# Optimization experiments

Hardware: AMD Instinct MI355X
Metric: run time of the kernel (lower is better)

The kernel has to match this reference:

```python
import jax, jax.numpy as jnp
import numpy as np

B, S, DIN, D, H, DK, FF, V, L = 4, 1024, 768, 224, 8, 28, 600, 8000, 8


def setup_inputs() -> dict:
    key = jax.random.key(0)
    ks = iter(jax.random.split(key, 32))
    g = lambda shape, s=0.02: jax.random.normal(next(ks), shape, jnp.float32) * s
    return {
        "x": jax.random.normal(next(ks), (B, S, DIN), jnp.float32),
        "Wp": g((DIN, D)), "bp": jnp.zeros((D,), jnp.float32),
        # per-layer stacked params, leading axis = L layers
        "Wq": g((L, H, D, DK)), "bq": jnp.zeros((L, H, DK), jnp.float32),
        "Wk": g((L, H, D, DK)), "bk": jnp.zeros((L, H, DK), jnp.float32),
        "Wv": g((L, H, D, DK)), "bv": jnp.zeros((L, H, DK), jnp.float32),
        "Wo": g((L, D, D)), "bo": jnp.zeros((L, D), jnp.float32),
        "W1": g((L, D, FF)), "b1": jnp.zeros((L, FF), jnp.float32),
        "W2": g((L, FF, FF)), "b2": jnp.zeros((L, FF), jnp.float32),
        "W3": g((L, FF, D)), "b3": jnp.zeros((L, D), jnp.float32),
        # LayerNorm over last TWO dims (seq, dmodel), one shared instance per layer
        "lnw": jnp.ones((L, S, D), jnp.float32), "lnb": jnp.zeros((L, S, D), jnp.float32),
        "Wf": g((D, V)), "bf": jnp.zeros((V,), jnp.float32),
    }


def _pos_enc(S_, D_):
    pos = jnp.arange(S_, dtype=jnp.float32)[:, None]          # [S,1]
    i = jnp.arange(D_, dtype=jnp.float32)[None, :]            # [1,D]
    ang = pos / jnp.power(jnp.float32(10000.0), 2.0 * i / D_)  # uses 2*i for BOTH
    return jnp.where(jnp.arange(D_)[None, :] % 2 == 0, jnp.sin(ang), jnp.cos(ang))


def _ln2d(x, w, b):
    # LayerNorm over last two dims (seq, dmodel), eps=1e-5
    mu = jnp.mean(x, axis=(-2, -1), keepdims=True)
    var = jnp.var(x, axis=(-2, -1), keepdims=True)
    return (x - mu) / jnp.sqrt(var + 1e-5) * w + b


def _attn(x, Wq, bq, Wk, bk, Wv, bv, Wo, bo):
    q = jnp.einsum('bsd,hdk->bhsk', x, Wq) + bq[:, None, :]
    k = jnp.einsum('bsd,hdk->bhsk', x, Wk) + bk[:, None, :]
    v = jnp.einsum('bsd,hdk->bhsk', x, Wv) + bv[:, None, :]
    scores = jnp.einsum('bhqk,bhsk->bhqs', q, k) / jnp.sqrt(jnp.float32(DK))
    causal = jnp.tril(jnp.ones((S, S), bool))
    scores = jnp.where(causal, scores, -jnp.inf)
    a = jax.nn.softmax(scores, axis=-1)
    o = jnp.einsum('bhqs,bhsk->bqhk', a, v).reshape(x.shape[0], S, D)
    return o @ Wo + bo + x  # residual inside attention (as in source)


def reference(x, Wp, bp, Wq, bq, Wk, bk, Wv, bv, Wo, bo,
              W1, b1, W2, b2, W3, b3, lnw, lnb, Wf, bf):
    h = x @ Wp + bp                      # proj_to_224: [B,S,224]
    h = h + _pos_enc(S, D)[None]         # positional encoding
    for l in range(L):
        h = _attn(h, Wq[l], bq[l], Wk[l], bk[l], Wv[l], bv[l], Wo[l], bo[l])
        h = _ln2d(h, lnw[l], lnb[l])
        f = jax.nn.relu(h @ W1[l] + b1[l])
        f = jax.nn.relu(f @ W2[l] + b2[l])
        f = f @ W3[l] + b3[l]
        h = _ln2d(f + h, lnw[l], lnb[l])  # feed_forward's LN (same params)
        h = _ln2d(h, lnw[l], lnb[l])      # outer LN (same params again)
    logits = (h @ Wf + bf) / 1.0          # temperature = 1.0
    return jax.nn.softmax(logits, axis=2)
```

## Files before the change

### kernel.cpp

```cpp
#include <hip/hip_runtime.h>
#include <math.h>

#define GF_BIAS   1
#define GF_RELU   2
#define GF_RESID  4
#define GF_POSENC 8
#define GF_F32OUT 16
#define GF_STAT6  32
#define GF_SWAP   64
#define GF_LNA    128
#define GF_LNA2   256
#define GF_LNRES  512
#define GF_LNRES2 1024

namespace {
constexpr int BB = 4, SS = 1024, DD = 224, FFF = 600, VV = 8000, LLl = 8;
constexpr int SD = SS * DD;
constexpr float INV_SD = 1.0f / (float)SD;

constexpr size_t WP   = 0;
constexpr size_t WQKV = WP + (size_t)256 * 768;
constexpr size_t WO   = WQKV + (size_t)LLl * 704 * 256;
constexpr size_t W1T  = WO + (size_t)LLl * 256 * 256;
constexpr size_t W2T  = W1T + (size_t)LLl * 640 * 256;
constexpr size_t W3T  = W2T + (size_t)LLl * 640 * 640;
constexpr size_t WFT  = W3T + (size_t)LLl * 256 * 640;
constexpr size_t HB   = WFT + (size_t)8064 * 256;
constexpr size_t H2B  = HB + (size_t)4096 * 256;
constexpr size_t OBUF = H2B + (size_t)4096 * 256;
constexpr size_t BIG  = OBUF + (size_t)4096 * 256;
constexpr size_t ENDB = BIG + (size_t)2 * 4096 * 640;
constexpr size_t FBYTE = ENDB * 2;
}

using short8 = __attribute__((ext_vector_type(8))) short;
using f32x4  = __attribute__((ext_vector_type(4))) float;

__device__ __forceinline__ float bits2f(unsigned u) {
  union { unsigned u; float f; } v; v.u = u; return v.f;
}
__device__ __forceinline__ unsigned short f2b(float f) {
  union { float f; unsigned u; } v; v.f = f;
  unsigned r = v.u + 0x7FFFu + ((v.u >> 16) & 1u);
  return (unsigned short)(r >> 16);
}
__device__ __forceinline__ float b2f(unsigned short b) {
  return bits2f((unsigned)b << 16);
}

__device__ __forceinline__ uint4 ln8(uint4 raw, const float* __restrict__ wp,
                                     const float* __restrict__ bp,
                                     float mu1, float rs1, float mu2, float rs2,
                                     bool dbl) {
  float4 w0 = *(const float4*)wp, w1v = *(const float4*)(wp + 4);
  float4 b0 = *(const float4*)bp, b1v = *(const float4*)(bp + 4);
  float wv[8] = {w0.x, w0.y, w0.z, w0.w, w1v.x, w1v.y, w1v.z, w1v.w};
  float bv[8] = {b0.x, b0.y, b0.z, b0.w, b1v.x, b1v.y, b1v.z, b1v.w};
  const unsigned* u = (const unsigned*)&raw;
  uint4 out;
  unsigned* ou = (unsigned*)&out;
#pragma unroll
  for (int q = 0; q < 4; ++q) {
    float x0 = bits2f(u[q] << 16), x1 = bits2f(u[q] & 0xFFFF0000u);
    float y0 = (x0 - mu1) * rs1 * wv[q * 2] + bv[q * 2];
    float y1 = (x1 - mu1) * rs1 * wv[q * 2 + 1] + bv[q * 2 + 1];
    if (dbl) {
      y0 = (y0 - mu2) * rs2 * wv[q * 2] + bv[q * 2];
      y1 = (y1 - mu2) * rs2 * wv[q * 2 + 1] + bv[q * 2 + 1];
    }
    ou[q] = (unsigned)f2b(y0) | ((unsigned)f2b(y1) << 16);
  }
  return out;
}

template <int BM, int BN, int FLAGS>
__global__ __launch_bounds__(256) void gemm_mfma(
    const unsigned short* __restrict__ A, const unsigned short* __restrict__ Bt,
    const float* __restrict__ bias, const unsigned short* __restrict__ Rz,
    void* __restrict__ Cout, int Kp, int N, int ldc,
    const float* __restrict__ lnwT, const float* __restrict__ lnbT,
    const float* __restrict__ stIn, const float* __restrict__ cst,
    const float* __restrict__ lnwS, const float* __restrict__ lnbS,
    float* __restrict__ statOut)
{
  constexpr bool HASLNA = (FLAGS & (GF_LNA | GF_LNA2)) != 0;
  constexpr bool HASLNR = (FLAGS & (GF_LNRES | GF_LNRES2)) != 0;
  constexpr bool DBLA = (FLAGS & GF_LNA2) != 0;
  constexpr bool DBLR = (FLAGS & GF_LNRES2) != 0;
  constexpr int MR = BM / 32, NR = BN / 32;
  constexpr int APT = BM / 32, BPT = BN / 32;
  constexpr int ABY = BM * 128, BBY = BN * 128;
  constexpr int CBY = (FLAGS & GF_F32OUT) ? (64 * (BN + 4) * 4) : (BM * (BN + 8) * 2);
  constexpr int SBY = (ABY + BBY) > CBY ? (ABY + BBY) : CBY;
  __shared__ __align__(16) char smem[SBY];
  __shared__ float red6[24];
  unsigned short* sA = (unsigned short*)smem;
  unsigned short* sB = (unsigned short*)(smem + ABY);
  const int t = threadIdx.x;
  const int l = t & 63;
  const int w = t >> 6, wr = w >> 1, wc = w & 1;
  const int m0 = ((FLAGS & GF_SWAP) ? blockIdx.x : blockIdx.y) * BM;
  const int n0 = ((FLAGS & GF_SWAP) ? blockIdx.y : blockIdx.x) * BN;
  const int nk = Kp >> 6;

  float mu1 = 0.f, rs1 = 1.f, mu2 = 0.f, rs2 = 1.f;
  if constexpr (HASLNA || HASLNR) {
    const float* st = stIn + (m0 >> 10) * 6;
    const float s0 = st[0], s1 = st[1];
    mu1 = s0 * INV_SD;
    rs1 = rsqrtf(s1 * INV_SD - mu1 * mu1 + 1e-5f);
    if constexpr (DBLA || DBLR) {
      const float swx = st[2], sw2x = st[3], sw2x2 = st[4], swbx = st[5];
      mu2 = (rs1 * (swx - mu1 * cst[0]) + cst[2]) * INV_SD;
      const float ey2 = (rs1 * rs1 * (sw2x2 - 2.f * mu1 * sw2x + mu1 * mu1 * cst[1]) +
                         2.f * rs1 * (swbx - mu1 * cst[4]) + cst[3]) * INV_SD;
      rs2 = rsqrtf(ey2 - mu2 * mu2 + 1e-5f);
    }
  }

  int aoff[APT], ar[APT], ac[APT];
#pragma unroll
  for (int p = 0; p < APT; ++p) {
    int off = (t + p * 256) * 16;
    int r = off >> 7;
    int cb = (off & 127) ^ ((r & 7) << 4);
    aoff[p] = off; ar[p] = r; ac[p] = cb >> 1;
  }
  int boff[BPT], br[BPT], bc[BPT];
#pragma unroll
  for (int p = 0; p < BPT; ++p) {
    int off = (t + p * 256) * 16;
    int r = off >> 7;
    int cb = (off & 127) ^ ((r & 7) << 4);
    boff[p] = off; br[p] = r; bc[p] = cb >> 1;
  }

  const unsigned short* Ab = A + (size_t)m0 * Kp;
  const unsigned short* Bb = Bt + (size_t)n0 * Kp;

  auto loadA = [&](int p, int kb) -> uint4 {
    const int d0 = kb + ac[p];
    uint4 raw = *(const uint4*)(Ab + (size_t)ar[p] * Kp + d0);
    if constexpr (HASLNA) {
      if (d0 >= DD) return make_uint4(0u, 0u, 0u, 0u);
      const int srow = (m0 + ar[p]) & (SS - 1);
      raw = ln8(raw, lnwT + (size_t)srow * DD + d0, lnbT + (size_t)srow * DD + d0,
                mu1, rs1, mu2, rs2, DBLA);
    }
    return raw;
  };

  uint4 ra[APT], rb[BPT];
#pragma unroll
  for (int p = 0; p < APT; ++p) ra[p] = loadA(p, 0);
#pragma unroll
  for (int p = 0; p < BPT; ++p) rb[p] = *(const uint4*)(Bb + (size_t)br[p] * Kp + bc[p]);

  f32x4 acc[MR][NR];
#pragma unroll
  for (int i = 0; i < MR; ++i)
#pragma unroll
    for (int j = 0; j < NR; ++j) acc[i][j] = {0.f, 0.f, 0.f, 0.f};

  for (int kt = 0; kt < nk; ++kt) {
#pragma unroll
    for (int p = 0; p < APT; ++p) *(uint4*)((char*)sA + aoff[p]) = ra[p];
#pragma unroll
    for (int p = 0; p < BPT; ++p) *(uint4*)((char*)sB + boff[p]) = rb[p];
    __syncthreads();
    if (kt + 1 < nk) {
      const int k1 = (kt + 1) * 64;
#pragma unroll
      for (int p = 0; p < APT; ++p) ra[p] = loadA(p, k1);
#pragma unroll
      for (int p = 0; p < BPT; ++p) rb[p] = *(const uint4*)(Bb + (size_t)br[p] * Kp + k1 + bc[p]);
    }
#pragma unroll
    for (int kh = 0; kh < 2; ++kh) {
      short8 af[MR], bfg[NR];
#pragma unroll
      for (int mi = 0; mi < MR; ++mi) {
        const int row = wr * (BM / 2) + mi * 16 + (l & 15);
        const int byte = (row * 128 + kh * 64 + (l >> 4) * 16) ^ ((row & 7) << 4);
        af[mi] = *(const short8*)((const char*)sA + byte);
      }
#pragma unroll
      for (int ni = 0; ni < NR; ++ni) {
        const int row = wc * (BN / 2) + ni * 16 + (l & 15);
        const int byte = (row * 128 + kh * 64 + (l >> 4) * 16) ^ ((row & 7) << 4);
        bfg[ni] = *(const short8*)((const char*)sB + byte);
      }
#pragma unroll
      for (int mi = 0; mi < MR; ++mi)
#pragma unroll
        for (int ni = 0; ni < NR; ++ni)
          acc[mi][ni] = __builtin_amdgcn_mfma_f32_16x16x32_bf16(af[mi], bfg[ni], acc[mi][ni], 0, 0, 0);
    }
    __syncthreads();
  }

  const int cl = l & 15, rl0 = (l >> 4) * 4;

  if constexpr ((FLAGS & GF_F32OUT) != 0) {
    constexpr int CST = BN + 4;
    float* Cs = (float*)smem;
    constexpr int NCH = BM / 64;
#pragma unroll
    for (int c = 0; c < NCH; ++c) {
      __syncthreads();
      if ((wr * (BM / 2)) / 64 == c) {
#pragma unroll
        for (int mi = 0; mi < MR; ++mi)
#pragma unroll
          for (int ni = 0; ni < NR; ++ni)
#pragma unroll
            for (int j = 0; j < 4; ++j) {
              const int rl = wr * (BM / 2) + mi * 16 + rl0 + j - c * 64;
              const int cc = wc * (BN / 2) + ni * 16 + cl;
              const int gn = n0 + cc;
              float v = acc[mi][ni][j];
              if ((FLAGS & GF_BIAS) && gn < N) v += bias[gn];
              Cs[rl * CST + cc] = v;
            }
      }
      __syncthreads();
      constexpr int CPR = BN / 4;
      constexpr int NIT = (64 * CPR) / 256;
#pragma unroll
      for (int i = 0; i < NIT; ++i) {
        const int ch = i * 256 + t;
        const int rr = ch / CPR, c4 = ch % CPR;
        const int gn = n0 + c4 * 4;
        const size_t gmr = (size_t)(m0 + c * 64 + rr);
        if (gn + 3 < N) {
          *(float4*)&((float*)Cout)[gmr * ldc + gn] = *(const float4*)&Cs[rr * CST + c4 * 4];
        } else {
#pragma unroll
          for (int c2 = 0; c2 < 4; ++c2)
            if (gn + c2 < N) ((float*)Cout)[gmr * ldc + gn + c2] = Cs[rr * CST + c4 * 4 + c2];
        }
      }
    }
  } else {
    constexpr int CST = BN + 8;
    unsigned short* Cs = (unsigned short*)smem;
    float ls0 = 0.f, ls1 = 0.f, ls2 = 0.f, ls3 = 0.f, ls4 = 0.f, ls5 = 0.f;
#pragma unroll
    for (int mi = 0; mi < MR; ++mi)
#pragma unroll
      for (int ni = 0; ni < NR; ++ni)
#pragma unroll
        for (int j = 0; j < 4; ++j) {
          const int rl = wr * (BM / 2) + mi * 16 + rl0 + j;
          const int cc = wc * (BN / 2) + ni * 16 + cl;
          const int gm = m0 + rl, gn = n0 + cc;
          const int srow = gm & (SS - 1);
          float v = acc[mi][ni][j];
          if ((FLAGS & GF_BIAS) && gn < N) v += bias[gn];
          if constexpr ((FLAGS & GF_RESID) != 0) {
            if constexpr (HASLNR) {
              if (gn < N) {
                float rv = b2f(Rz[(size_t)gm * ldc + gn]);
                const float wE = lnwT[(size_t)srow * DD + gn];
                const float bE = lnbT[(size_t)srow * DD + gn];
                rv = (rv - mu1) * rs1 * wE + bE;
                if constexpr (DBLR) rv = (rv - mu2) * rs2 * wE + bE;
                v += rv;
              }
            } else {
              v += b2f(Rz[(size_t)gm * ldc + gn]);
            }
          }
          if ((FLAGS & GF_POSENC) && gn < N) {
            float freq = expf(-(2.0f * gn / 224.0f) * 9.210340371976184f);
            float ang = (float)srow * freq;
            v += (gn & 1) ? cosf(ang) : sinf(ang);
          }
          if (FLAGS & GF_RELU) v = fmaxf(v, 0.f);
          if constexpr ((FLAGS & GF_STAT6) != 0) {
            if (gn < N) {
              const float wS = lnwS[(size_t)srow * DD + gn];
              const float bS = lnbS[(size_t)srow * DD + gn];
              const float wv = wS * v;
              ls0 += v; ls1 += v * v; ls2 += wv; ls3 += wS * wv;
              ls4 += wv * wv; ls5 += bS * wv;
            }
          }
          Cs[rl * CST + cc] = f2b(v);
        }
    __syncthreads();
#pragma unroll
    for (int it = 0; it < BM / 32; ++it) {
      const int rr = it * 32 + (t >> 3), qq = t & 7;
      const size_t gm = (size_t)(m0 + rr);
      *(uint4*)&((unsigned short*)Cout)[gm * ldc + n0 + qq * 8] =
          *(const uint4*)&Cs[rr * CST + qq * 8];
    }
    if constexpr ((FLAGS & GF_STAT6) != 0) {
      float s[6] = {ls0, ls1, ls2, ls3, ls4, ls5};
#pragma unroll
      for (int o2 = 32; o2 > 0; o2 >>= 1)
#pragma unroll
        for (int j = 0; j < 6; ++j) s[j] += __shfl_down(s[j], o2);
      if (l == 0)
#pragma unroll
        for (int j = 0; j < 6; ++j) red6[w * 6 + j] = s[j];
      __syncthreads();
      if (t < 6) {
        const float tot = red6[t] + red6[6 + t] + red6[12 + t] + red6[18 + t];
        atomicAdd(&statOut[(m0 >> 10) * 6 + t], tot);
      }
    }
  }
}

__global__ void zero_stats(float* __restrict__ st)
{
  if (threadIdx.x < 424) st[threadIdx.x] = 0.f;
}

__global__ __launch_bounds__(256) void lnconst(const float* __restrict__ lnw,
                                               const float* __restrict__ lnb,
                                               float* __restrict__ cst)
{
  const int ll = blockIdx.y, g = blockIdx.x;
  const float* wv = lnw + (size_t)ll * SD + g * 3584;
  const float* bv = lnb + (size_t)ll * SD + g * 3584;
  float s[5] = {0.f, 0.f, 0.f, 0.f, 0.f};
  for (int c = threadIdx.x * 4; c < 3584; c += 1024) {
    float4 w4 = *(const float4*)(wv + c);
    float4 b4 = *(const float4*)(bv + c);
    const float* wf = (const float*)&w4;
    const float* bf2 = (const float*)&b4;
#pragma unroll
    for (int e = 0; e < 4; ++e) {
      const float ww = wf[e], bb = bf2[e];
      s[0] += ww; s[1] += ww * ww; s[2] += bb; s[3] += bb * bb; s[4] += ww * bb;
    }
  }
#pragma unroll
  for (int o2 = 32; o2 > 0; o2 >>= 1)
#pragma unroll
    for (int j = 0; j < 5; ++j) s[j] += __shfl_down(s[j], o2);
  __shared__ float red[4][5];
  if ((threadIdx.x & 63) == 0)
#pragma unroll
    for (int j = 0; j < 5; ++j) red[threadIdx.x >> 6][j] = s[j];
  __syncthreads();
  if (threadIdx.x < 5) {
    const float tot = red[0][threadIdx.x] + red[1][threadIdx.x] +
                      red[2][threadIdx.x] + red[3][threadIdx.x];
    atomicAdd(&cst[ll * 5 + threadIdx.x], tot);
  }
}

__global__ __launch_bounds__(256) void ln2mat(
    const unsigned short* __restrict__ X, const float* __restrict__ lnw,
    const float* __restrict__ lnb, const float* __restrict__ st,
    const float* __restrict__ cst, unsigned short* __restrict__ Y)
{
  const int chunk = blockIdx.x * 256 + threadIdx.x;
  const int r = chunk >> 5, cc = chunk & 31;
  if (cc >= 28) {
    *(uint4*)(Y + (size_t)r * 256 + cc * 8) = make_uint4(0u, 0u, 0u, 0u);
    return;
  }
  const int b = r >> 10, srow = r & 1023;
  const float* s = st + b * 6;
  const float mu1 = s[0] * INV_SD;
  const float rs1 = rsqrtf(s[1] * INV_SD - mu1 * mu1 + 1e-5f);
  const float mu2 = (rs1 * (s[2] - mu1 * cst[0]) + cst[2]) * INV_SD;
  const float ey2 = (rs1 * rs1 * (s[4] - 2.f * mu1 * s[3] + mu1 * mu1 * cst[1]) +
                     2.f * rs1 * (s[5] - mu1 * cst[4]) + cst[3]) * INV_SD;
  const float rs2 = rsqrtf(ey2 - mu2 * mu2 + 1e-5f);
  uint4 raw = *(const uint4*)(X + (size_t)r * 256 + cc * 8);
  uint4 out = ln8(raw, lnw + (size_t)srow * DD + cc * 8, lnb + (size_t)srow * DD + cc * 8,
                  mu1, rs1, mu2, rs2, true);
  *(uint4*)(Y + (size_t)r * 256 + cc * 8) = out;
}

__global__ __launch_bounds__(256) void prep_wt2(
    const float* __restrict__ W, unsigned short* __restrict__ O,
    int K, int N, int Kp, int Np, size_t sW, size_t sO)
{
  const int ll = blockIdx.y;
  const int tx = Np >> 5;
  const int tn = blockIdx.x % tx, tk = blockIdx.x / tx;
  const int n0 = tn * 32, k0 = tk * 32;
  const float* Wl = W + sW * ll;
  unsigned short* Ol = O + sO * ll;
  __shared__ float T[32][36];
  {
    const int r = threadIdx.x >> 3, c4 = (threadIdx.x & 7) * 4;
    const int k = k0 + r, n = n0 + c4;
    float4 v = make_float4(0.f, 0.f, 0.f, 0.f);
    if (k < K) {
      if (n + 3 < N) v = *(const float4*)&Wl[(size_t)k * N + n];
      else {
        if (n + 0 < N) v.x = Wl[(size_t)k * N + n + 0];
        if (n + 1 < N) v.y = Wl[(size_t)k * N + n + 1];
        if (n + 2 < N) v.z = Wl[(size_t)k * N + n + 2];
        if (n + 3 < N) v.w = Wl[(size_t)k * N + n + 3];
      }
    }
    *(float4*)&T[r][c4] = v;
  }
  __syncthreads();
  {
    const int nl = threadIdx.x >> 3, k4 = (threadIdx.x & 7) * 4;
    ushort4 u;
    u.x = f2b(T[k4 + 0][nl]); u.y = f2b(T[k4 + 1][nl]);
    u.z = f2b(T[k4 + 2][nl]); u.w = f2b(T[k4 + 3][nl]);
    *(ushort4*)&Ol[(size_t)(n0 + nl) * Kp + k0 + k4] = u;
  }
}

__global__ void prep_wqkv(const float* __restrict__ Wq, const float* __restrict__ Wk,
                          const float* __restrict__ Wv, const float* __restrict__ bq,
                          const float* __restrict__ bk, const float* __restrict__ bv,
                          unsigned short* __restrict__ O, float* __restrict__ bcat)
{
  const int idx = blockIdx.x * 256 + threadIdx.x;
  if (idx < LLl * 8 * 224 * 28) {
    const int kk = idx % 28;
    const int d  = (idx / 28) % 224;
    const int h  = (idx / (28 * 224)) % 8;
    const int ll = idx / (28 * 224 * 8);
    const int col = h * 28 + kk;
    const size_t base = (size_t)ll * (704 * 256);
    O[base + (size_t)col * 256 + d]         = f2b(Wq[idx]);
    O[base + (size_t)(224 + col) * 256 + d] = f2b(Wk[idx]);
    O[base + (size_t)(448 + col) * 256 + d] = f2b(Wv[idx]);
  }
  if (idx < LLl * 8 * 28) {
    const int kk = idx % 28;
    const int h  = (idx / 28) % 8;
    const int ll = idx / (28 * 8);
    const int col = h * 28 + kk;
    bcat[ll * 672 + col]       = bq[idx];
    bcat[ll * 672 + 224 + col] = bk[idx];
    bcat[ll * 672 + 448 + col] = bv[idx];
  }
}

__global__ void prep_x(const float* __restrict__ x, unsigned short* __restrict__ xb)
{
  const size_t i = ((size_t)blockIdx.x * 256 + threadIdx.x) * 4;
  float4 v = *(const float4*)(x + i);
  ushort4 o;
  o.x = f2b(v.x); o.y = f2b(v.y); o.z = f2b(v.z); o.w = f2b(v.w);
  *(ushort4*)(xb + i) = o;
}

__global__ __launch_bounds__(256) void attn_mfma(const unsigned short* __restrict__ qkv,
                                                 unsigned short* __restrict__ o)
{
  const int bh = blockIdx.x;
  const int qt = (int)gridDim.y - 1 - (int)blockIdx.y;
  const int b = bh >> 3, h = bh & 7;
  const int tid = threadIdx.x;
  const int w = tid >> 6, l = tid & 63;
  const int cl = l & 15, g = l >> 4;
  const int qbase = qt * 64 + w * 16;
  const float scale = 0.1889822365046136f;

  __shared__ unsigned short Ks[32 * 40];
  __shared__ unsigned short Vt[32 * 40];
  __shared__ unsigned short Ps[4][16 * 40];

  short8 aq;
  {
    const unsigned short* qp = qkv + ((size_t)(b * SS + qbase + cl)) * 704 + h * 28;
#pragma unroll
    for (int e = 0; e < 8; ++e) {
      const int d = g * 8 + e;
      ((unsigned short*)&aq)[e] = (d < 28) ? qp[d] : (unsigned short)0;
    }
  }

  f32x4 o0 = {0.f, 0.f, 0.f, 0.f}, o1 = {0.f, 0.f, 0.f, 0.f};
  float m[4] = {-INFINITY, -INFINITY, -INFINITY, -INFINITY};
  float lsum[4] = {0.f, 0.f, 0.f, 0.f};

  const int ntiles = qt * 2 + 2;
  const int ntw = ((qbase + 15) >> 5) + 1;

  const int sr = tid >> 3, sc4 = (tid & 7) << 2;
  const bool sact = (sc4 < 28);
  ushort4 ku = make_ushort4(0, 0, 0, 0), vu = make_ushort4(0, 0, 0, 0);
  if (sact) {
    const unsigned short* kp = qkv + ((size_t)(b * SS + sr)) * 704 + 224 + h * 28 + sc4;
    ku = *(const ushort4*)kp;
    vu = *(const ushort4*)(kp + 224);
  }

  for (int tile = 0; tile < ntiles; ++tile) {
    const int t0 = tile * 32;
    __syncthreads();
    *(ushort4*)&Ks[sr * 40 + sc4] = ku;
    Vt[(sc4 + 0) * 40 + sr] = vu.x;
    Vt[(sc4 + 1) * 40 + sr] = vu.y;
    Vt[(sc4 + 2) * 40 + sr] = vu.z;
    Vt[(sc4 + 3) * 40 + sr] = vu.w;
    __syncthreads();
    if (tile + 1 < ntiles && sact) {
      const unsigned short* kp =
          qkv + ((size_t)(b * SS + (tile + 1) * 32 + sr)) * 704 + 224 + h * 28 + sc4;
      ku = *(const ushort4*)kp;
      vu = *(const ushort4*)(kp + 224);
    }
    if (tile >= ntw) continue;

    const short8 bk0 = *(const short8*)&Ks[cl * 40 + g * 8];
    const short8 bk1 = *(const short8*)&Ks[(cl + 16) * 40 + g * 8];
    f32x4 zz = {0.f, 0.f, 0.f, 0.f};
    f32x4 s0 = __builtin_amdgcn_mfma_f32_16x16x32_bf16(aq, bk0, zz, 0, 0, 0);
    f32x4 s1 = __builtin_amdgcn_mfma_f32_16x16x32_bf16(aq, bk1, zz, 0, 0, 0);

    const bool diag = (t0 + 31 > qbase);
#pragma unroll
    for (int jj = 0; jj < 4; ++jj) {
      float v0 = s0[jj] * scale, v1 = s1[jj] * scale;
      if (diag) {
        const int qr = qbase + g * 4 + jj;
        if (t0 + cl > qr)      v0 = -INFINITY;
        if (t0 + 16 + cl > qr) v1 = -INFINITY;
      }
      float rm = fmaxf(v0, v1);
      rm = fmaxf(rm, __shfl_xor(rm, 1));
      rm = fmaxf(rm, __shfl_xor(rm, 2));
      rm = fmaxf(rm, __shfl_xor(rm, 4));
      rm = fmaxf(rm, __shfl_xor(rm, 8));
      const float mnew = fmaxf(m[jj], rm);
      const float r2 = __expf(m[jj] - mnew);
      m[jj] = mnew;
      const float e0 = __expf(v0 - mnew), e1 = __expf(v1 - mnew);
      lsum[jj] = lsum[jj] * r2 + e0 + e1;
      o0[jj] *= r2; o1[jj] *= r2;
      Ps[w][(g * 4 + jj) * 40 + cl]      = f2b(e0);
      Ps[w][(g * 4 + jj) * 40 + cl + 16] = f2b(e1);
    }
    const short8 pa  = *(const short8*)&Ps[w][cl * 40 + g * 8];
    const short8 bv0 = *(const short8*)&Vt[cl * 40 + g * 8];
    const short8 bv1 = *(const short8*)&Vt[(cl + 16) * 40 + g * 8];
    o0 = __builtin_amdgcn_mfma_f32_16x16x32_bf16(pa, bv0, o0, 0, 0, 0);
    o1 = __builtin_amdgcn_mfma_f32_16x16x32_bf16(pa, bv1, o1, 0, 0, 0);
  }

#pragma unroll
  for (int jj = 0; jj < 4; ++jj) {
    float ls = lsum[jj];
    ls += __shfl_xor(ls, 1);
    ls += __shfl_xor(ls, 2);
    ls += __shfl_xor(ls, 4);
    ls += __shfl_xor(ls, 8);
    const float inv = 1.0f / ls;
    const int row = qbase + g * 4 + jj;
    unsigned short* op = o + ((size_t)(b * SS + row)) * 256 + h * 28;
    op[cl] = f2b(o0[jj] * inv);
    if (cl < 12) op[16 + cl] = f2b(o1[jj] * inv);
  }
}

__global__ __launch_bounds__(256) void softmax_rows(float* __restrict__ logits)
{
  const int row = blockIdx.x;
  float* p = logits + (size_t)row * VV;
  __shared__ float buf[VV];
  __shared__ float red[4];
  const int tid = threadIdx.x;

  float mx = -INFINITY;
  for (int i = tid; i < VV; i += 256) { float v = p[i]; buf[i] = v; mx = fmaxf(mx, v); }
#pragma unroll
  for (int o2 = 32; o2 > 0; o2 >>= 1) mx = fmaxf(mx, __shfl_down(mx, o2));
  if ((tid & 63) == 0) red[tid >> 6] = mx;
  __syncthreads();
  mx = fmaxf(fmaxf(red[0], red[1]), fmaxf(red[2], red[3]));
  __syncthreads();

  float s = 0.f;
  for (int i = tid; i < VV; i += 256) { float e = __expf(buf[i] - mx); buf[i] = e; s += e; }
#pragma unroll
  for (int o2 = 32; o2 > 0; o2 >>= 1) s += __shfl_down(s, o2);
  if ((tid & 63) == 0) red[tid >> 6] = s;
  __syncthreads();
  s = red[0] + red[1] + red[2] + red[3];
  const float inv = 1.0f / s;
  for (int i = tid; i < VV; i += 256) p[i] = buf[i] * inv;
}

extern "C" void kernel_launch(void* const* d_in, const int* in_sizes, int n_in,
                              void* d_out, int out_size, void* d_ws, size_t ws_size,
                              hipStream_t stream) {
  const float* x   = (const float*)d_in[0];
  const float* Wp  = (const float*)d_in[1];
  const float* bp  = (const float*)d_in[2];
  const float* Wq  = (const float*)d_in[3];
  const float* bq  = (const float*)d_in[4];
  const float* Wk  = (const float*)d_in[5];
  const float* bk  = (const float*)d_in[6];
  const float* Wv  = (const float*)d_in[7];
  const float* bv  = (const float*)d_in[8];
  const float* Wo  = (const float*)d_in[9];
  const float* bo  = (const float*)d_in[10];
  const float* W1  = (const float*)d_in[11];
  const float* b1  = (const float*)d_in[12];
  const float* W2  = (const float*)d_in[13];
  const float* b2  = (const float*)d_in[14];
  const float* W3  = (const float*)d_in[15];
  const float* b3  = (const float*)d_in[16];
  const float* lnw = (const float*)d_in[17];
  const float* lnb = (const float*)d_in[18];
  const float* Wf  = (const float*)d_in[19];
  const float* bf  = (const float*)d_in[20];

  unsigned short* wsb = (unsigned short*)d_ws;
  unsigned short* wpT   = wsb + WP;
  unsigned short* wqkvT = wsb + WQKV;
  unsigned short* woT   = wsb + WO;
  unsigned short* w1T   = wsb + W1T;
  unsigned short* w2T   = wsb + W2T;
  unsigned short* w3T   = wsb + W3T;
  unsigned short* wfT   = wsb + WFT;
  unsigned short* X     = wsb + HB;
  unsigned short* h2a   = wsb + H2B;
  unsigned short* obuf  = wsb + OBUF;
  unsigned short* xb    = wsb + BIG;
  unsigned short* qkvb  = wsb + BIG;
  unsigned short* f1    = wsb + BIG;
  unsigned short* f2    = wsb + BIG + (size_t)4096 * 640;
  float* bcat  = (float*)((char*)d_ws + FBYTE);
  float* stats = bcat + LLl * 672;
  float* cstA  = stats + 384;

  zero_stats<<<1, 512, 0, stream>>>(stats);
  lnconst<<<dim3(64, LLl), 256, 0, stream>>>(lnw, lnb, cstA);
  hipMemsetAsync(wqkvT, 0, (size_t)LLl * 704 * 256 * 2, stream);
  prep_x<<<3072, 256, 0, stream>>>(x, xb);
  prep_wt2<<<dim3(192, 1), 256, 0, stream>>>(Wp, wpT, 768, 224, 768, 256, 0, 0);
  prep_wqkv<<<dim3(1568, 1), 256, 0, stream>>>(Wq, Wk, Wv, bq, bk, bv, wqkvT, bcat);
  prep_wt2<<<dim3(64, 8), 256, 0, stream>>>(Wo, woT, 224, 224, 256, 256,
                                            (size_t)224 * 224, (size_t)256 * 256);
  prep_wt2<<<dim3(160, 8), 256, 0, stream>>>(W1, w1T, 224, 600, 256, 640,
                                             (size_t)224 * 600, (size_t)640 * 256);
  prep_wt2<<<dim3(400, 8), 256, 0, stream>>>(W2, w2T, 600, 600, 640, 640,
                                             (size_t)600 * 600, (size_t)640 * 640);
  prep_wt2<<<dim3(160, 8), 256, 0, stream>>>(W3, w3T, 600, 224, 640, 256,
                                             (size_t)600 * 224, (size_t)256 * 640);
  prep_wt2<<<dim3(2016, 1), 256, 0, stream>>>(Wf, wfT, 224, 8000, 256, 8064, 0, 0);

  gemm_mfma<32, 64, GF_BIAS | GF_POSENC><<<dim3(4, 128), 256, 0, stream>>>(
      xb, wpT, bp, nullptr, X, 768, 224, 256,
      nullptr, nullptr, nullptr, nullptr, nullptr, nullptr, nullptr);

  for (int l = 0; l < LLl; ++l) {
    float* stA = stats + (size_t)(2 * l) * 24;
    float* stB = stats + (size_t)(2 * l + 1) * 24;
    const float* stPrev = stats + (size_t)(2 * l - 1) * 24;
    const float* lnwP = lnw + (size_t)(l - 1) * SD;
    const float* lnbP = lnb + (size_t)(l - 1) * SD;
    const float* cstP = cstA + (l - 1) * 5;
    const float* lnwL = lnw + (size_t)l * SD;
    const float* lnbL = lnb + (size_t)l * SD;

    if (l == 0) {
      gemm_mfma<64, 64, GF_BIAS><<<dim3(11, 64), 256, 0, stream>>>(
          X, wqkvT, bcat, nullptr, qkvb, 256, 672, 704,
          nullptr, nullptr, nullptr, nullptr, nullptr, nullptr, nullptr);
    } else {
      gemm_mfma<64, 64, GF_BIAS | GF_LNA2><<<dim3(11, 64), 256, 0, stream>>>(
          X, wqkvT + (size_t)l * 704 * 256, bcat + l * 672, nullptr, qkvb, 256, 672, 704,
          lnwP, lnbP, stPrev, cstP, nullptr, nullptr, nullptr);
    }
    attn_mfma<<<dim3(BB * 8, SS / 64), 256, 0, stream>>>(qkvb, obuf);
    if (l == 0) {
      gemm_mfma<32, 64, GF_BIAS | GF_RESID | GF_STAT6><<<dim3(4, 128), 256, 0, stream>>>(
          obuf, woT, bo, X, h2a, 256, 224, 256,
          nullptr, nullptr, nullptr, nullptr, lnwL, lnbL, stA);
    } else {
      gemm_mfma<32, 64, GF_BIAS | GF_RESID | GF_LNRES2 | GF_STAT6>
          <<<dim3(4, 128), 256, 0, stream>>>(
          obuf, woT + (size_t)l * 256 * 256, bo + (size_t)l * 224, X, h2a, 256, 224, 256,
          lnwP, lnbP, stPrev, cstP, lnwL, lnbL, stA);
    }
    gemm_mfma<64, 64, GF_BIAS | GF_RELU | GF_LNA><<<dim3(10, 64), 256, 0, stream>>>(
        h2a, w1T + (size_t)l * 640 * 256, b1 + (size_t)l * 600, nullptr, f1, 256, 600, 640,
        lnwL, lnbL, stA, nullptr, nullptr, nullptr, nullptr);
    gemm_mfma<64, 64, GF_BIAS | GF_RELU><<<dim3(10, 64), 256, 0, stream>>>(
        f1, w2T + (size_t)l * 640 * 640, b2 + (size_t)l * 600, nullptr, f2, 640, 600, 640,
        nullptr, nullptr, nullptr, nullptr, nullptr, nullptr, nullptr);
    gemm_mfma<32, 64, GF_BIAS | GF_RESID | GF_LNRES | GF_STAT6>
        <<<dim3(4, 128), 256, 0, stream>>>(
        f2, w3T + (size_t)l * 256 * 640, b3 + (size_t)l * 224, h2a, X, 640, 224, 256,
        lnwL, lnbL, stA, nullptr, lnwL, lnbL, stB);
  }

  ln2mat<<<512, 256, 0, stream>>>(X, lnw + (size_t)7 * SD, lnb + (size_t)7 * SD,
                                  stats + (size_t)15 * 24, cstA + 7 * 5, h2a);
  gemm_mfma<128, 128, GF_BIAS | GF_F32OUT | GF_SWAP><<<dim3(32, 63), 256, 0, stream>>>(
      h2a, wfT, bf, nullptr, (float*)d_out, 256, 8000, 8000,
      nullptr, nullptr, nullptr, nullptr, nullptr, nullptr, nullptr);
  softmax_rows<<<4096, 256, 0, stream>>>((float*)d_out);
}
```

Before: 1.342 ms.

## Fuse the three FFN GEMMs into one kernel keeping intermediates in LDS

Replaces the three separate FFN GEMM launches (W1+ReLU, W2+ReLU, W3+residual+LN stats) with one kernel. Each block handles 16 rows and keeps the f1/f2 activations in shared memory, so the two intermediate global round trips and two launches go away. In exchange, every block streams the full W1/W2/W3 weight matrices directly from global/L2 with no LDS tiling, and only 256 blocks of 16 rows are launched, which may limit MFMA utilisation and make the kernel weight-bandwidth bound.

```diff
diff --git a/kernel.cpp b/kernel.cpp
--- a/kernel.cpp
+++ b/kernel.cpp
@@ -314,6 +314,142 @@
   }
 }
 
+__global__ __launch_bounds__(256) void ffn_fused(
+    const unsigned short* __restrict__ h2a,
+    const unsigned short* __restrict__ W1t, const unsigned short* __restrict__ W2t,
+    const unsigned short* __restrict__ W3t,
+    const float* __restrict__ b1, const float* __restrict__ b2,
+    const float* __restrict__ b3,
+    const float* __restrict__ lnw, const float* __restrict__ lnb,
+    const float* __restrict__ stA, float* __restrict__ statOut,
+    unsigned short* __restrict__ Xout)
+{
+  __shared__ __align__(16) unsigned short sA[16 * 280];
+  __shared__ __align__(16) unsigned short f1s[16 * 648];
+  __shared__ __align__(16) unsigned short f2s[16 * 648];
+  __shared__ float red6[24];
+  const int t = threadIdx.x;
+  const int l = t & 63, w = t >> 6;
+  const int cl = l & 15, g8 = (l >> 4) * 8, rl0 = (l >> 4) * 4;
+  const int m0 = blockIdx.x * 16;
+  const float* st = stA + (m0 >> 10) * 6;
+  const float mu1 = st[0] * INV_SD;
+  const float rs1 = rsqrtf(st[1] * INV_SD - mu1 * mu1 + 1e-5f);
+
+  for (int c = t; c < 512; c += 256) {
+    const int r = c >> 5, col = (c & 31) * 8;
+    uint4 v = make_uint4(0u, 0u, 0u, 0u);
+    if (col < DD) {
+      const int srow = (m0 + r) & (SS - 1);
+      uint4 raw = *(const uint4*)(h2a + (size_t)(m0 + r) * 256 + col);
+      v = ln8(raw, lnw + (size_t)srow * DD + col, lnb + (size_t)srow * DD + col,
+              mu1, rs1, 0.f, 1.f, false);
+    }
+    *(uint4*)(sA + r * 280 + col) = v;
+  }
+  __syncthreads();
+
+  {
+    f32x4 acc[10];
+#pragma unroll
+    for (int i = 0; i < 10; ++i) acc[i] = {0.f, 0.f, 0.f, 0.f};
+    for (int ks = 0; ks < 8; ++ks) {
+      const short8 af = *(const short8*)(sA + cl * 280 + ks * 32 + g8);
+#pragma unroll
+      for (int ni = 0; ni < 10; ++ni) {
+        const int n = w * 160 + ni * 16 + cl;
+        const short8 bf = *(const short8*)(W1t + (size_t)n * 256 + ks * 32 + g8);
+        acc[ni] = __builtin_amdgcn_mfma_f32_16x16x32_bf16(af, bf, acc[ni], 0, 0, 0);
+      }
+    }
+#pragma unroll
+    for (int ni = 0; ni < 10; ++ni) {
+      const int col = w * 160 + ni * 16 + cl;
+      const float bias = (col < FFF) ? b1[col] : 0.f;
+#pragma unroll
+      for (int j = 0; j < 4; ++j)
+        f1s[(rl0 + j) * 648 + col] = f2b(fmaxf(acc[ni][j] + bias, 0.f));
+    }
+  }
+  __syncthreads();
+
+  {
+    f32x4 acc[10];
+#pragma unroll
+    for (int i = 0; i < 10; ++i) acc[i] = {0.f, 0.f, 0.f, 0.f};
+    for (int ks = 0; ks < 20; ++ks) {
+      const short8 af = *(const short8*)(f1s + cl * 648 + ks * 32 + g8);
+#pragma unroll
+      for (int ni = 0; ni < 10; ++ni) {
+        const int n = w * 160 + ni * 16 + cl;
+        const short8 bf = *(const short8*)(W2t + (size_t)n * 640 + ks * 32 + g8);
+        acc[ni] = __builtin_amdgcn_mfma_f32_16x16x32_bf16(af, bf, acc[ni], 0, 0, 0);
+      }
+    }
+#pragma unroll
+    for (int ni = 0; ni < 10; ++ni) {
+      const int col = w * 160 + ni * 16 + cl;
+      const float bias = (col < FFF) ? b2[col] : 0.f;
+#pragma unroll
+      for (int j = 0; j < 4; ++j)
+        f2s[(rl0 + j) * 648 + col] = f2b(fmaxf(acc[ni][j] + bias, 0.f));
+    }
+  }
+  __syncthreads();
+
+  float s6[6] = {0.f, 0.f, 0.f, 0.f, 0.f, 0.f};
+  {
+    f32x4 acc[4];
+#pragma unroll
+    for (int i = 0; i < 4; ++i) acc[i] = {0.f, 0.f, 0.f, 0.f};
+    for (int ks = 0; ks < 20; ++ks) {
+      const short8 af = *(const short8*)(f2s + cl * 648 + ks * 32 + g8);
+#pragma unroll
+      for (int ni = 0; ni < 4; ++ni) {
+        const int n = w * 64 + ni * 16 + cl;
+        const short8 bf = *(const short8*)(W3t + (size_t)n * 640 + ks * 32 + g8);
+        acc[ni] = __builtin_amdgcn_mfma_f32_16x16x32_bf16(af, bf, acc[ni], 0, 0, 0);
+      }
+    }
+    unsigned short* Cs = sA;
+#pragma unroll
+    for (int ni = 0; ni < 4; ++ni) {
+      const int col = w * 64 + ni * 16 + cl;
+      const float bias = (col < DD) ? b3[col] : 0.f;
+#pragma unroll
+      for (int j = 0; j < 4; ++j) {
+        const int gm = m0 + rl0 + j;
+        const int srow = gm & (SS - 1);
+        float v = acc[ni][j] + bias;
+        if (col < DD) {
+          const float wE = lnw[(size_t)srow * DD + col];
+          const float bE = lnb[(size_t)srow * DD + col];
+          v += (b2f(h2a[(size_t)gm * 256 + col]) - mu1) * rs1 * wE + bE;
+          const float wv = wE * v;
+          s6[0] += v; s6[1] += v * v; s6[2] += wv; s6[3] += wE * wv;
+          s6[4] += wv * wv; s6[5] += bE * wv;
+        }
+        Cs[(rl0 + j) * 280 + col] = f2b(v);
+      }
+    }
+  }
+#pragma unroll
+  for (int o2 = 32; o2 > 0; o2 >>= 1)
+#pragma unroll
+    for (int j2 = 0; j2 < 6; ++j2) s6[j2] += __shfl_down(s6[j2], o2);
+  if (l == 0)
+#pragma unroll
+    for (int j2 = 0; j2 < 6; ++j2) red6[w * 6 + j2] = s6[j2];
+  __syncthreads();
+  if (t < 6)
+    atomicAdd(&statOut[(m0 >> 10) * 6 + t],
+              red6[t] + red6[6 + t] + red6[12 + t] + red6[18 + t]);
+  for (int c = t; c < 512; c += 256) {
+    const int r = c >> 5, col = (c & 31) * 8;
+    *(uint4*)(Xout + (size_t)(m0 + r) * 256 + col) = *(const uint4*)(sA + r * 280 + col);
+  }
+}
+
 __global__ void zero_stats(float* __restrict__ st)
 {
   if (threadIdx.x < 424) st[threadIdx.x] = 0.f;
@@ -628,8 +764,6 @@
   unsigned short* obuf  = wsb + OBUF;
   unsigned short* xb    = wsb + BIG;
   unsigned short* qkvb  = wsb + BIG;
-  unsigned short* f1    = wsb + BIG;
-  unsigned short* f2    = wsb + BIG + (size_t)4096 * 640;
   float* bcat  = (float*)((char*)d_ws + FBYTE);
   float* stats = bcat + LLl * 672;
   float* cstA  = stats + 384;
@@ -684,16 +818,10 @@
           obuf, woT + (size_t)l * 256 * 256, bo + (size_t)l * 224, X, h2a, 256, 224, 256,
           lnwP, lnbP, stPrev, cstP, lnwL, lnbL, stA);
     }
-    gemm_mfma<64, 64, GF_BIAS | GF_RELU | GF_LNA><<<dim3(10, 64), 256, 0, stream>>>(
-        h2a, w1T + (size_t)l * 640 * 256, b1 + (size_t)l * 600, nullptr, f1, 256, 600, 640,
-        lnwL, lnbL, stA, nullptr, nullptr, nullptr, nullptr);
-    gemm_mfma<64, 64, GF_BIAS | GF_RELU><<<dim3(10, 64), 256, 0, stream>>>(
-        f1, w2T + (size_t)l * 640 * 640, b2 + (size_t)l * 600, nullptr, f2, 640, 600, 640,
-        nullptr, nullptr, nullptr, nullptr, nullptr, nullptr, nullptr);
-    gemm_mfma<32, 64, GF_BIAS | GF_RESID | GF_LNRES | GF_STAT6>
-        <<<dim3(4, 128), 256, 0, stream>>>(
-        f2, w3T + (size_t)l * 256 * 640, b3 + (size_t)l * 224, h2a, X, 640, 224, 256,
-        lnwL, lnbL, stA, nullptr, lnwL, lnbL, stB);
+    ffn_fused<<<256, 256, 0, stream>>>(
+        h2a, w1T + (size_t)l * 640 * 256, w2T + (size_t)l * 640 * 640,
+        w3T + (size_t)l * 256 * 640, b1 + (size_t)l * 600, b2 + (size_t)l * 600,
+        b3 + (size_t)l * 224, lnwL, lnbL, stA, stB, X);
   }
 
   ln2mat<<<512, 256, 0, stream>>>(X, lnw + (size_t)7 * SD, lnb + (size_t)7 * SD,
```

After: 1.274 ms. 5.1% less time.
